# Kernel tuning notes

Hardware: AMD Instinct MI355X
Metric: run time of the kernel (lower is better)

## Reference

```python
import jax, jax.numpy as jnp
import numpy as np

INPUT_DIM = 1024
NUM_CLASSES = 1024
NUM_EXPERTS = 8
TOP_K = 2
HIDDEN = 128  # hard-coded in Expert


def setup_inputs() -> dict:
    key = jax.random.key(0)
    ks = jax.random.split(key, 7)
    s = 0.02
    return {
        "x": jax.random.normal(ks[0], (16384, INPUT_DIM), dtype=jnp.float32),
        "gate_w": jax.random.normal(ks[1], (INPUT_DIM, NUM_EXPERTS), dtype=jnp.float32) * s,
        "gate_b": jnp.zeros((NUM_EXPERTS,), dtype=jnp.float32),
        "w1": jax.random.normal(ks[2], (NUM_EXPERTS, INPUT_DIM, HIDDEN), dtype=jnp.float32) * s,
        "b1": jnp.zeros((NUM_EXPERTS, HIDDEN), dtype=jnp.float32),
        "w2": jax.random.normal(ks[3], (NUM_EXPERTS, HIDDEN, NUM_CLASSES), dtype=jnp.float32) * s,
        "b2": jnp.zeros((NUM_EXPERTS, NUM_CLASSES), dtype=jnp.float32),
    }


def reference(x, gate_w, gate_b, w1, b1, w2, b2):
    B = x.shape[0]
    # gating: softmax over experts, then top-k
    scores = jax.nn.softmax(x @ gate_w + gate_b, axis=1)          # [B, E]
    top_vals, top_idx = jax.lax.top_k(scores, TOP_K)              # [B, K]
    # dense all-expert compute (E small, fixed), then gather selected outputs
    h = jax.nn.relu(jnp.einsum('bi,eih->ebh', x, w1) + b1[:, None, :])   # [E, B, H]
    y = jnp.einsum('ebh,ehc->ebc', h, w2) + b2[:, None, :]               # [E, B, C]
    y = jnp.transpose(y, (1, 0, 2))                                      # [B, E, C]
    sel = jnp.take_along_axis(y, top_idx[:, :, None], axis=1)            # [B, K, C]
    output = jnp.sum(top_vals[:, :, None] * sel, axis=1)                 # [B, C]
    # gates expanded to [B, K, C] then summed over batch -> [K, C]
    gates_sum = jnp.broadcast_to(jnp.sum(top_vals, axis=0)[:, None], (TOP_K, NUM_CLASSES))
    return (output, gates_sum)
```

## Files before the change

kernel.cpp:

```cpp
#include <hip/hip_runtime.h>

#define B_ROWS  16384
#define IN_DIM  1024
#define NEXP    8
#define HID     128
#define NCLS    1024
#define NPAIR   56
#define MAXW1   520
#define MAXW2   312

#define GATE_BLOCKS (B_ROWS / 8)
#define W1T_BLOCKS  (NEXP * (IN_DIM / 32) * (HID / 32))
#define W2T_BLOCKS  (NEXP * (HID / 32) * (NCLS / 32))

typedef __attribute__((ext_vector_type(8))) short bf16x8;
typedef __attribute__((ext_vector_type(4))) float f32x4;
typedef __attribute__((ext_vector_type(4))) unsigned int u32x4;
typedef __attribute__((ext_vector_type(8))) unsigned short u16x8;

__device__ __forceinline__ unsigned short f2bf(float f) {
  union { float f; unsigned u; } v; v.f = f;
  unsigned r = v.u + 0x7FFFu + ((v.u >> 16) & 1u);
  return (unsigned short)(r >> 16);
}

__device__ __forceinline__ int sw64(int row, int sh) {
  return (row << 6) + ((((sh >> 3) ^ row) & 7) << 3) + (sh & 7);
}
__device__ __forceinline__ int sw256(int row, int sh) {
  return (row << 8) + ((((sh >> 3) ^ row) & 7) << 3) + (sh & 7) + ((sh >> 6) << 6);
}

__global__ __launch_bounds__(256) void prep_kernel(
    const float* __restrict__ x, const float* __restrict__ gw,
    const float* __restrict__ gb, const float* __restrict__ w1,
    const float* __restrict__ w2, unsigned short* __restrict__ xb,
    unsigned short* __restrict__ w1bt, unsigned short* __restrict__ w2bt,
    float2* __restrict__ tval, unsigned char* __restrict__ pairid) {
  __shared__ __attribute__((aligned(16))) unsigned char pmem[NEXP * IN_DIM * 4];
  const int bid = blockIdx.x;
  const int t = threadIdx.x;

  if (bid < GATE_BLOCKS) {
    float (*gws)[IN_DIM] = (float(*)[IN_DIM])pmem;
#pragma unroll
    for (int kk = 0; kk < 4; ++kk) {
      const int k = kk * 256 + t;
      const float4 g0 = *(const float4*)(gw + k * NEXP);
      const float4 g1 = *(const float4*)(gw + k * NEXP + 4);
      gws[0][k] = g0.x; gws[1][k] = g0.y; gws[2][k] = g0.z; gws[3][k] = g0.w;
      gws[4][k] = g1.x; gws[5][k] = g1.y; gws[6][k] = g1.z; gws[7][k] = g1.w;
    }
    __syncthreads();

    const int wave = t >> 6, l = t & 63;
    const int r0 = bid * 8 + wave * 2;

    float4 xv0[4], xv1[4];
#pragma unroll
    for (int j = 0; j < 4; ++j) {
      xv0[j] = *(const float4*)(x + (size_t)r0 * IN_DIM + j * 256 + l * 4);
      xv1[j] = *(const float4*)(x + (size_t)(r0 + 1) * IN_DIM + j * 256 + l * 4);
    }

    if (xb) {
#pragma unroll
      for (int j = 0; j < 4; ++j) {
        uint2 p0, p1;
        p0.x = (unsigned)f2bf(xv0[j].x) | ((unsigned)f2bf(xv0[j].y) << 16);
        p0.y = (unsigned)f2bf(xv0[j].z) | ((unsigned)f2bf(xv0[j].w) << 16);
        p1.x = (unsigned)f2bf(xv1[j].x) | ((unsigned)f2bf(xv1[j].y) << 16);
        p1.y = (unsigned)f2bf(xv1[j].z) | ((unsigned)f2bf(xv1[j].w) << 16);
        *(uint2*)(xb + (size_t)r0 * IN_DIM + j * 256 + l * 4)       = p0;
        *(uint2*)(xb + (size_t)(r0 + 1) * IN_DIM + j * 256 + l * 4) = p1;
      }
    }

    float a0[NEXP], a1[NEXP];
#pragma unroll
    for (int e = 0; e < NEXP; ++e) { a0[e] = 0.f; a1[e] = 0.f; }
#pragma unroll
    for (int e = 0; e < NEXP; ++e) {
#pragma unroll
      for (int j = 0; j < 4; ++j) {
        const float4 g = *(const float4*)&gws[e][j * 256 + l * 4];
        a0[e] = fmaf(xv0[j].x, g.x, a0[e]); a0[e] = fmaf(xv0[j].y, g.y, a0[e]);
        a0[e] = fmaf(xv0[j].z, g.z, a0[e]); a0[e] = fmaf(xv0[j].w, g.w, a0[e]);
        a1[e] = fmaf(xv1[j].x, g.x, a1[e]); a1[e] = fmaf(xv1[j].y, g.y, a1[e]);
        a1[e] = fmaf(xv1[j].z, g.z, a1[e]); a1[e] = fmaf(xv1[j].w, g.w, a1[e]);
      }
    }
#pragma unroll
    for (int e = 0; e < NEXP; ++e) {
#pragma unroll
      for (int off = 32; off > 0; off >>= 1) {
        a0[e] += __shfl_xor(a0[e], off);
        a1[e] += __shfl_xor(a1[e], off);
      }
    }

    if (l == 0) {
#pragma unroll
      for (int rr = 0; rr < 2; ++rr) {
        const float* a = rr ? a1 : a0;
        float lg[NEXP];
#pragma unroll
        for (int e = 0; e < NEXP; ++e) lg[e] = a[e] + gb[e];
        float m = lg[0];
#pragma unroll
        for (int e = 1; e < NEXP; ++e) m = fmaxf(m, lg[e]);
        float p[NEXP], s = 0.f;
#pragma unroll
        for (int e = 0; e < NEXP; ++e) { p[e] = __expf(lg[e] - m); s += p[e]; }
        const float inv = 1.f / s;
        int   i0 = 0;  float v0 = p[0];
#pragma unroll
        for (int e = 1; e < NEXP; ++e) if (p[e] > v0) { v0 = p[e]; i0 = e; }
        int   i1 = -1; float v1 = -1.f;
#pragma unroll
        for (int e = 0; e < NEXP; ++e)
          if (e != i0 && p[e] > v1) { v1 = p[e]; i1 = e; }
        tval[r0 + rr] = make_float2(v0 * inv, v1 * inv);
        pairid[r0 + rr] = (unsigned char)(i0 * 7 + i1 - (i1 > i0 ? 1 : 0));
      }
    }
  } else {
    float (*tile)[33] = (float(*)[33])pmem;
    const float* src; unsigned short* dst;
    int R, C, r0, c0, e;
    if (bid < GATE_BLOCKS + W1T_BLOCKS) {
      const int b1 = bid - GATE_BLOCKS;
      e = b1 >> 7; const int rem = b1 & 127;
      R = IN_DIM; C = HID;
      c0 = (rem & 3) * 32; r0 = (rem >> 2) * 32;
      src = w1; dst = w1bt;
    } else {
      const int b2 = bid - GATE_BLOCKS - W1T_BLOCKS;
      e = b2 >> 7; const int rem = b2 & 127;
      R = HID; C = NCLS;
      c0 = (rem & 31) * 32; r0 = (rem >> 5) * 32;
      src = w2; dst = w2bt;
    }
    src += (size_t)e * R * C;
    dst += (size_t)e * R * C;
    const int tx = t & 31, ty = t >> 5;
#pragma unroll
    for (int i = ty; i < 32; i += 8)
      tile[i][tx] = src[(size_t)(r0 + i) * C + c0 + tx];
    __syncthreads();
#pragma unroll
    for (int i = ty; i < 32; i += 8)
      dst[(size_t)(c0 + i) * R + r0 + tx] = f2bf(tile[tx][i]);
  }
}

__global__ __launch_bounds__(256) void hist_part_kernel(
    const unsigned char* __restrict__ pairid, const float2* __restrict__ tval,
    int* __restrict__ partials, float2* __restrict__ psum) {
  __shared__ int h[64];
  __shared__ float s0a[256], s1a[256];
  const int t = threadIdx.x;
  if (t < 64) h[t] = 0;
  __syncthreads();
  const int row = blockIdx.x * 256 + t;
  const int p  = pairid[row];
  const int ea = p / 7, rem = p % 7;
  const int eb = rem + (rem >= ea ? 1 : 0);
  atomicAdd(&h[p], 1);
  atomicAdd(&h[56 + ea], 1);
  atomicAdd(&h[56 + eb], 1);
  const float2 v = tval[row];
  s0a[t] = v.x; s1a[t] = v.y;
  __syncthreads();
#pragma unroll
  for (int s = 128; s > 0; s >>= 1) {
    if (t < s) { s0a[t] += s0a[t + s]; s1a[t] += s1a[t + s]; }
    __syncthreads();
  }
  if (t < 64) partials[blockIdx.x * 64 + t] = h[t];
  if (t == 0) psum[blockIdx.x] = make_float2(s0a[0], s1a[0]);
}

__global__ void scan_kernel(const int* __restrict__ partials,
                            const float2* __restrict__ psum,
                            int* __restrict__ hist, int* __restrict__ base,
                            int* __restrict__ csr, int* __restrict__ meta,
                            float* __restrict__ out) {
  const int t = threadIdx.x;
  __shared__ float gg[2];
  if (t < 64) {
    int s = 0;
    for (int b = 0; b < B_ROWS / 256; ++b) s += partials[b * 64 + t];
    hist[t] = s;
  }
  if (t == 0) {
    float g0 = 0.f, g1 = 0.f;
    for (int b = 0; b < B_ROWS / 256; ++b) { g0 += psum[b].x; g1 += psum[b].y; }
    gg[0] = g0; gg[1] = g1;
  }
  __syncthreads();
  float* gout = out + (size_t)B_ROWS * NCLS;
  for (int c = t; c < NCLS; c += 64) {
    gout[c]        = gg[0];
    gout[NCLS + c] = gg[1];
  }
  if (t != 0) return;
  int accp = 0, acce = 0;
  for (int p = 0; p < NPAIR; ++p) { base[p] = accp; csr[p] = accp; accp += hist[p]; }
  for (int e = 0; e < NEXP; ++e) {
    base[56 + e] = acce; csr[56 + e] = acce; acce += hist[56 + e];
  }
  int n = 0;
  int* w1 = meta + 2;
  for (int e = 0; e < NEXP; ++e) {
    const int tiles = (hist[56 + e] + 63) >> 6;
    for (int i = 0; i < tiles; ++i) w1[n++] = (e << 16) | i;
  }
  meta[0] = n;
  n = 0;
  int* w2 = meta + 2 + MAXW1;
  for (int p = 0; p < NPAIR; ++p) {
    const int tiles = (hist[p] + 63) >> 6;
    for (int i = 0; i < tiles; ++i) w2[n++] = (p << 16) | i;
  }
  meta[1] = n;
}

__global__ __launch_bounds__(256) void scatter_kernel(
    const unsigned char* __restrict__ pairid, int* __restrict__ csr,
    int* __restrict__ elist, int* __restrict__ plist) {
  __shared__ int h[64], lbase[64];
  const int t = threadIdx.x;
  if (t < 64) h[t] = 0;
  __syncthreads();
  const int row = blockIdx.x * 256 + t;
  const int p  = pairid[row];
  const int ea = p / 7, rem = p % 7;
  const int eb = rem + (rem >= ea ? 1 : 0);
  const int op = atomicAdd(&h[p], 1);
  const int oa = atomicAdd(&h[56 + ea], 1);
  const int ob = atomicAdd(&h[56 + eb], 1);
  __syncthreads();
  if (t < 64) lbase[t] = h[t] ? atomicAdd(&csr[t], h[t]) : 0;
  __syncthreads();
  const int pp = lbase[p] + op;
  plist[pp] = row;
  elist[lbase[56 + ea] + oa] = (pp << 15) | (row << 1);
  elist[lbase[56 + eb] + ob] = (pp << 15) | (row << 1) | 1;
}

template <bool XB>
__global__ __launch_bounds__(256) void k1_hidden(
    const float* __restrict__ x, const unsigned short* __restrict__ xb,
    const unsigned short* __restrict__ w1bt, const float* __restrict__ b1,
    const float2* __restrict__ tval, const int* __restrict__ elist,
    const int* __restrict__ hist, const int* __restrict__ base,
    const int* __restrict__ meta, unsigned short* __restrict__ Hg) {
  const int b = blockIdx.x;
  if (b >= meta[0]) return;
  const int item = meta[2 + b];
  const int e = item >> 16, tile = item & 0xffff;
  const int start = tile * 64;
  const int nr = min(64, hist[56 + e] - start);

  __shared__ unsigned short As[64 * 64];
  __shared__ unsigned short Bs[128 * 64];
  __shared__ int rowl[64];

  const int t = threadIdx.x;
  if (t < 64) rowl[t] = elist[base[56 + e] + start + (t < nr ? t : 0)];
  __syncthreads();

  const int wid = t >> 6, l = t & 63;
  const int wr = wid >> 1, wc = wid & 1;
  const int lg = l >> 4,   ln = l & 15;

  f32x4 acc[2][4];
#pragma unroll
  for (int ms = 0; ms < 2; ++ms)
#pragma unroll
    for (int nf = 0; nf < 4; ++nf) acc[ms][nf] = (f32x4){0.f, 0.f, 0.f, 0.f};

  const int ai = t >> 2, aseg = t & 3;
  const int arow = (rowl[ai] >> 1) & 0x3FFF;
  const float* asrcf = x + (size_t)arow * IN_DIM + aseg * 16;
  const unsigned short* asrcb = xb + (size_t)arow * IN_DIM + aseg * 16;
  const int bn = t >> 1, bhf = t & 1;
  const unsigned short* bsrc =
      w1bt + ((size_t)e * HID + bn) * IN_DIM + bhf * 32;

  if constexpr (XB) {
    u32x4 areg[2], breg[4];
    {
      const u32x4* ap = (const u32x4*)(asrcb);
      areg[0] = ap[0]; areg[1] = ap[1];
      const u32x4* bp = (const u32x4*)(bsrc);
#pragma unroll
      for (int j = 0; j < 4; ++j) breg[j] = bp[j];
    }
    for (int ks = 0; ks < 16; ++ks) {
      *(u32x4*)&As[sw64(ai, aseg * 16)]     = areg[0];
      *(u32x4*)&As[sw64(ai, aseg * 16 + 8)] = areg[1];
#pragma unroll
      for (int j = 0; j < 4; ++j)
        *(u32x4*)&Bs[sw64(bn, bhf * 32 + j * 8)] = breg[j];
      __syncthreads();
      if (ks < 15) {
        const u32x4* ap = (const u32x4*)(asrcb + (ks + 1) * 64);
        areg[0] = ap[0]; areg[1] = ap[1];
        const u32x4* bp = (const u32x4*)(bsrc + (ks + 1) * 64);
#pragma unroll
        for (int j = 0; j < 4; ++j) breg[j] = bp[j];
      }
      bf16x8 af[2][2], bf[4][2];
#pragma unroll
      for (int ms = 0; ms < 2; ++ms)
#pragma unroll
        for (int kh = 0; kh < 2; ++kh)
          af[ms][kh] = *(const bf16x8*)&As[sw64(wr*32 + ms*16 + ln, kh*32 + lg*8)];
#pragma unroll
      for (int nf = 0; nf < 4; ++nf)
#pragma unroll
        for (int kh = 0; kh < 2; ++kh)
          bf[nf][kh] = *(const bf16x8*)&Bs[sw64(wc*64 + nf*16 + ln, kh*32 + lg*8)];
#pragma unroll
      for (int ms = 0; ms < 2; ++ms)
#pragma unroll
        for (int nf = 0; nf < 4; ++nf) {
          acc[ms][nf] = __builtin_amdgcn_mfma_f32_16x16x32_bf16(af[ms][0], bf[nf][0], acc[ms][nf], 0, 0, 0);
          acc[ms][nf] = __builtin_amdgcn_mfma_f32_16x16x32_bf16(af[ms][1], bf[nf][1], acc[ms][nf], 0, 0, 0);
        }
      __syncthreads();
    }
  } else {
    for (int ks = 0; ks < 16; ++ks) {
      {
        const float4 f0 = *(const float4*)(asrcf + ks * 64);
        const float4 f1 = *(const float4*)(asrcf + ks * 64 + 4);
        const float4 f2 = *(const float4*)(asrcf + ks * 64 + 8);
        const float4 f3 = *(const float4*)(asrcf + ks * 64 + 12);
        u16x8 u0, u1;
        u0[0]=f2bf(f0.x); u0[1]=f2bf(f0.y); u0[2]=f2bf(f0.z); u0[3]=f2bf(f0.w);
        u0[4]=f2bf(f1.x); u0[5]=f2bf(f1.y); u0[6]=f2bf(f1.z); u0[7]=f2bf(f1.w);
        u1[0]=f2bf(f2.x); u1[1]=f2bf(f2.y); u1[2]=f2bf(f2.z); u1[3]=f2bf(f2.w);
        u1[4]=f2bf(f3.x); u1[5]=f2bf(f3.y); u1[6]=f2bf(f3.z); u1[7]=f2bf(f3.w);
        *(u16x8*)&As[sw64(ai, aseg * 16)]     = u0;
        *(u16x8*)&As[sw64(ai, aseg * 16 + 8)] = u1;
      }
      {
        const u32x4* bp = (const u32x4*)(bsrc + ks * 64);
#pragma unroll
        for (int j = 0; j < 4; ++j)
          *(u32x4*)&Bs[sw64(bn, bhf * 32 + j * 8)] = bp[j];
      }
      __syncthreads();
      bf16x8 af[2][2], bf[4][2];
#pragma unroll
      for (int ms = 0; ms < 2; ++ms)
#pragma unroll
        for (int kh = 0; kh < 2; ++kh)
          af[ms][kh] = *(const bf16x8*)&As[sw64(wr*32 + ms*16 + ln, kh*32 + lg*8)];
#pragma unroll
      for (int nf = 0; nf < 4; ++nf)
#pragma unroll
        for (int kh = 0; kh < 2; ++kh)
          bf[nf][kh] = *(const bf16x8*)&Bs[sw64(wc*64 + nf*16 + ln, kh*32 + lg*8)];
#pragma unroll
      for (int ms = 0; ms < 2; ++ms)
#pragma unroll
        for (int nf = 0; nf < 4; ++nf) {
          acc[ms][nf] = __builtin_amdgcn_mfma_f32_16x16x32_bf16(af[ms][0], bf[nf][0], acc[ms][nf], 0, 0, 0);
          acc[ms][nf] = __builtin_amdgcn_mfma_f32_16x16x32_bf16(af[ms][1], bf[nf][1], acc[ms][nf], 0, 0, 0);
        }
      __syncthreads();
    }
  }

  float b1c[4];
#pragma unroll
  for (int nf = 0; nf < 4; ++nf) b1c[nf] = b1[e * HID + wc*64 + nf*16 + ln];

#pragma unroll
  for (int ms = 0; ms < 2; ++ms)
#pragma unroll
    for (int r = 0; r < 4; ++r) {
      const int li = wr*32 + ms*16 + lg*4 + r;
      if (li < nr) {
        const int packed = rowl[li];
        const int row  = (packed >> 1) & 0x3FFF;
        const int slot = packed & 1;
        const int pp   = ((unsigned)packed) >> 15;
        const float2 tv = tval[row];
        const float vv = slot ? tv.y : tv.x;
#pragma unroll
        for (int nf = 0; nf < 4; ++nf) {
          const float hh = fmaxf(acc[ms][nf][r] + b1c[nf], 0.f) * vv;
          Hg[((size_t)pp * 2 + slot) * HID + wc*64 + nf*16 + ln] = f2bf(hh);
        }
      }
    }
}

__global__ __launch_bounds__(256) void k2_out(
    const unsigned short* __restrict__ Hg, const unsigned short* __restrict__ w2bt,
    const float* __restrict__ b2, const float2* __restrict__ tval,
    const int* __restrict__ plist, const int* __restrict__ hist,
    const int* __restrict__ base, const int* __restrict__ meta,
    float* __restrict__ out) {
  const int b = blockIdx.y;
  if (b >= meta[1]) return;
  const int item = meta[2 + MAXW1 + b];
  const int p = item >> 16, rt = item & 0xffff;
  const int ea = p / 7, rem = p % 7;
  const int eb = rem + (rem >= ea ? 1 : 0);
  const int start = rt * 64;
  const int gpos = base[p] + start;
  const int nr = min(64, hist[p] - start);
  const int c0 = blockIdx.x * 128;

  __shared__ unsigned short Ah[64 * 256];
  __shared__ unsigned short Bs[128 * 64];
  __shared__ int rowl[64];
  __shared__ float2 vals[64];

  const int t = threadIdx.x;
  if (t < 64) {
    const int r = plist[gpos + (t < nr ? t : 0)];
    rowl[t] = r;
    vals[t] = tval[r];
  }
  __syncthreads();

  {
    const int i = t >> 2, q = t & 3;
    const int srow = min(gpos + i, B_ROWS - 1);
    const u32x4* src = (const u32x4*)(Hg + (size_t)srow * 256 + q * 64);
#pragma unroll
    for (int j = 0; j < 8; ++j)
      *(u32x4*)&Ah[sw256(i, q * 64 + j * 8)] = src[j];
  }

  const int wid = t >> 6, l = t & 63;
  const int wr = wid >> 1, wc = wid & 1;
  const int lg = l >> 4,   ln = l & 15;

  f32x4 acc[2][4];
#pragma unroll
  for (int ms = 0; ms < 2; ++ms)
#pragma unroll
    for (int nf = 0; nf < 4; ++nf) acc[ms][nf] = (f32x4){0.f, 0.f, 0.f, 0.f};

  const int bn = t >> 1, bhf = t & 1;
  u32x4 breg[4];
  {
    const u32x4* bp = (const u32x4*)(
        w2bt + ((size_t)ea * NCLS + c0 + bn) * HID + bhf * 32);
#pragma unroll
    for (int j = 0; j < 4; ++j) breg[j] = bp[j];
  }
#pragma unroll
  for (int ks = 0; ks < 4; ++ks) {
#pragma unroll
    for (int j = 0; j < 4; ++j)
      *(u32x4*)&Bs[sw64(bn, bhf * 32 + j * 8)] = breg[j];
    __syncthreads();
    if (ks < 3) {
      const int exn = (ks + 1 < 2) ? ea : eb;
      const int hbn = ((ks + 1) & 1) * 64;
      const u32x4* bp = (const u32x4*)(
          w2bt + ((size_t)exn * NCLS + c0 + bn) * HID + hbn + bhf * 32);
#pragma unroll
      for (int j = 0; j < 4; ++j) breg[j] = bp[j];
    }
    bf16x8 af[2][2], bf[4][2];
#pragma unroll
    for (int ms = 0; ms < 2; ++ms)
#pragma unroll
      for (int kh = 0; kh < 2; ++kh)
        af[ms][kh] = *(const bf16x8*)&Ah[sw256(wr*32 + ms*16 + ln, ks*64 + kh*32 + lg*8)];
#pragma unroll
    for (int nf = 0; nf < 4; ++nf)
#pragma unroll
      for (int kh = 0; kh < 2; ++kh)
        bf[nf][kh] = *(const bf16x8*)&Bs[sw64(wc*64 + nf*16 + ln, kh*32 + lg*8)];
#pragma unroll
    for (int ms = 0; ms < 2; ++ms)
#pragma unroll
      for (int nf = 0; nf < 4; ++nf) {
        acc[ms][nf] = __builtin_amdgcn_mfma_f32_16x16x32_bf16(af[ms][0], bf[nf][0], acc[ms][nf], 0, 0, 0);
        acc[ms][nf] = __builtin_amdgcn_mfma_f32_16x16x32_bf16(af[ms][1], bf[nf][1], acc[ms][nf], 0, 0, 0);
      }
    __syncthreads();
  }

  float b2a[4], b2b[4];
#pragma unroll
  for (int nf = 0; nf < 4; ++nf) {
    const int c = c0 + wc*64 + nf*16 + ln;
    b2a[nf] = b2[ea * NCLS + c];
    b2b[nf] = b2[eb * NCLS + c];
  }
#pragma unroll
  for (int ms = 0; ms < 2; ++ms)
#pragma unroll
    for (int r = 0; r < 4; ++r) {
      const int li = wr*32 + ms*16 + lg*4 + r;
      if (li < nr) {
        const int row = rowl[li];
        const float2 v = vals[li];
#pragma unroll
        for (int nf = 0; nf < 4; ++nf) {
          const int c = c0 + wc*64 + nf*16 + ln;
          out[(size_t)row * NCLS + c] = acc[ms][nf][r] + v.x * b2a[nf] + v.y * b2b[nf];
        }
      }
    }
}

extern "C" void kernel_launch(void* const* d_in, const int* in_sizes, int n_in,
                              void* d_out, int out_size, void* d_ws, size_t ws_size,
                              hipStream_t stream) {
  const float* x   = (const float*)d_in[0];
  const float* gw  = (const float*)d_in[1];
  const float* gb  = (const float*)d_in[2];
  const float* w1  = (const float*)d_in[3];
  const float* b1  = (const float*)d_in[4];
  const float* w2  = (const float*)d_in[5];
  const float* b2  = (const float*)d_in[6];
  float* out = (float*)d_out;

  char* ws = (char*)d_ws;
  int*            hist     = (int*)(ws);
  int*            base     = (int*)(ws + 256);
  int*            csr      = (int*)(ws + 512);
  int*            meta     = (int*)(ws + 768);
  int*            partials = (int*)(ws + 4352);
  float2*         psum     = (float2*)(ws + 20736);
  unsigned char*  pairid   = (unsigned char*)(ws + 21248);
  float2*         tval     = (float2*)(ws + 37632);
  int*            elist    = (int*)(ws + 168704);
  int*            plist    = (int*)(ws + 299776);
  unsigned short* w1bt     = (unsigned short*)(ws + 365312);
  unsigned short* w2bt     = (unsigned short*)(ws + 2462464);
  unsigned short* Hg       = (unsigned short*)(ws + 4559616);
  const bool use_xb = (ws_size >= (size_t)46502656);
  unsigned short* xb = use_xb ? (unsigned short*)(ws + 12948224) : nullptr;

  prep_kernel<<<GATE_BLOCKS + W1T_BLOCKS + W2T_BLOCKS, 256, 0, stream>>>(
      x, gw, gb, w1, w2, xb, w1bt, w2bt, tval, pairid);
  hist_part_kernel<<<B_ROWS / 256, 256, 0, stream>>>(pairid, tval, partials, psum);
  scan_kernel<<<1, 64, 0, stream>>>(partials, psum, hist, base, csr, meta, out);
  scatter_kernel<<<B_ROWS / 256, 256, 0, stream>>>(pairid, csr, elist, plist);

  if (use_xb)
    k1_hidden<true><<<MAXW1, 256, 0, stream>>>(x, xb, w1bt, b1, tval, elist,
                                               hist, base, meta, Hg);
  else
    k1_hidden<false><<<MAXW1, 256, 0, stream>>>(x, xb, w1bt, b1, tval, elist,
                                                hist, base, meta, Hg);
  k2_out<<<dim3(NCLS / 128, MAXW2), 256, 0, stream>>>(Hg, w2bt, b2, tval, plist,
                                                      hist, base, meta, out);
}
```

Measured before the change: 119.2 us.

## Fuse histogram into gating kernel, parallelize scan, widen k2 column tiles

Measured after the change: 187.4 us. 57.2% more time.

```diff
diff --git a/kernel.cpp b/kernel.cpp
--- a/kernel.cpp
+++ b/kernel.cpp
@@ -36,8 +36,11 @@
     const float* __restrict__ gb, const float* __restrict__ w1,
     const float* __restrict__ w2, unsigned short* __restrict__ xb,
     unsigned short* __restrict__ w1bt, unsigned short* __restrict__ w2bt,
-    float2* __restrict__ tval, unsigned char* __restrict__ pairid) {
+    float2* __restrict__ tval, unsigned char* __restrict__ pairid,
+    int* __restrict__ partials, float2* __restrict__ psum) {
   __shared__ __attribute__((aligned(16))) unsigned char pmem[NEXP * IN_DIM * 4];
+  __shared__ int hh[64];
+  __shared__ float ps[8];
   const int bid = blockIdx.x;
   const int t = threadIdx.x;
 
@@ -51,6 +54,7 @@
       gws[0][k] = g0.x; gws[1][k] = g0.y; gws[2][k] = g0.z; gws[3][k] = g0.w;
       gws[4][k] = g1.x; gws[5][k] = g1.y; gws[6][k] = g1.z; gws[7][k] = g1.w;
     }
+    if (t < 64) hh[t] = 0;
     __syncthreads();
 
     const int wave = t >> 6, l = t & 63;
@@ -100,6 +104,7 @@
     }
 
     if (l == 0) {
+      float sv0 = 0.f, sv1 = 0.f;
 #pragma unroll
       for (int rr = 0; rr < 2; ++rr) {
         const float* a = rr ? a1 : a0;
@@ -121,9 +126,21 @@
         for (int e = 0; e < NEXP; ++e)
           if (e != i0 && p[e] > v1) { v1 = p[e]; i1 = e; }
         tval[r0 + rr] = make_float2(v0 * inv, v1 * inv);
-        pairid[r0 + rr] = (unsigned char)(i0 * 7 + i1 - (i1 > i0 ? 1 : 0));
-      }
-    }
+        const int pr = i0 * 7 + i1 - (i1 > i0 ? 1 : 0);
+        pairid[r0 + rr] = (unsigned char)pr;
+        sv0 += v0 * inv; sv1 += v1 * inv;
+        atomicAdd(&hh[pr], 1);
+        atomicAdd(&hh[56 + i0], 1);
+        atomicAdd(&hh[56 + i1], 1);
+      }
+      ps[wave * 2]     = sv0;
+      ps[wave * 2 + 1] = sv1;
+    }
+    __syncthreads();
+    if (t < 64) partials[(size_t)bid * 64 + t] = hh[t];
+    if (t == 0)
+      psum[bid] = make_float2(ps[0] + ps[2] + ps[4] + ps[6],
+                              ps[1] + ps[3] + ps[5] + ps[7]);
   } else {
     float (*tile)[33] = (float(*)[33])pmem;
     const float* src; unsigned short* dst;
@@ -154,53 +171,39 @@
   }
 }
 
-__global__ __launch_bounds__(256) void hist_part_kernel(
-    const unsigned char* __restrict__ pairid, const float2* __restrict__ tval,
-    int* __restrict__ partials, float2* __restrict__ psum) {
-  __shared__ int h[64];
-  __shared__ float s0a[256], s1a[256];
+__global__ __launch_bounds__(256) void scan_kernel(
+    const int* __restrict__ partials, const float2* __restrict__ psum,
+    int* __restrict__ hist, int* __restrict__ base, int* __restrict__ csr,
+    int* __restrict__ meta, float* __restrict__ out) {
   const int t = threadIdx.x;
-  if (t < 64) h[t] = 0;
-  __syncthreads();
-  const int row = blockIdx.x * 256 + t;
-  const int p  = pairid[row];
-  const int ea = p / 7, rem = p % 7;
-  const int eb = rem + (rem >= ea ? 1 : 0);
-  atomicAdd(&h[p], 1);
-  atomicAdd(&h[56 + ea], 1);
-  atomicAdd(&h[56 + eb], 1);
-  const float2 v = tval[row];
-  s0a[t] = v.x; s1a[t] = v.y;
-  __syncthreads();
+  __shared__ int hpart[256];
+  __shared__ float r0a[256], r1a[256];
+  __shared__ float gg[2];
+
+  {
+    const int bin = t & 63, ch = t >> 6;
+    int s = 0;
+    for (int b = ch; b < GATE_BLOCKS; b += 4) s += partials[(size_t)b * 64 + bin];
+    hpart[t] = s;
+  }
+  {
+    float g0 = 0.f, g1 = 0.f;
+    for (int b = t; b < GATE_BLOCKS; b += 256) { g0 += psum[b].x; g1 += psum[b].y; }
+    r0a[t] = g0; r1a[t] = g1;
+  }
+  __syncthreads();
+  if (t < 64)
+    hist[t] = hpart[t] + hpart[64 + t] + hpart[128 + t] + hpart[192 + t];
 #pragma unroll
   for (int s = 128; s > 0; s >>= 1) {
-    if (t < s) { s0a[t] += s0a[t + s]; s1a[t] += s1a[t + s]; }
+    if (t < s) { r0a[t] += r0a[t + s]; r1a[t] += r1a[t + s]; }
     __syncthreads();
   }
-  if (t < 64) partials[blockIdx.x * 64 + t] = h[t];
-  if (t == 0) psum[blockIdx.x] = make_float2(s0a[0], s1a[0]);
-}
-
-__global__ void scan_kernel(const int* __restrict__ partials,
-                            const float2* __restrict__ psum,
-                            int* __restrict__ hist, int* __restrict__ base,
-                            int* __restrict__ csr, int* __restrict__ meta,
-                            float* __restrict__ out) {
-  const int t = threadIdx.x;
-  __shared__ float gg[2];
-  if (t < 64) {
-    int s = 0;
-    for (int b = 0; b < B_ROWS / 256; ++b) s += partials[b * 64 + t];
-    hist[t] = s;
-  }
-  if (t == 0) {
-    float g0 = 0.f, g1 = 0.f;
-    for (int b = 0; b < B_ROWS / 256; ++b) { g0 += psum[b].x; g1 += psum[b].y; }
-    gg[0] = g0; gg[1] = g1;
-  }
-  __syncthreads();
+  if (t == 0) { gg[0] = r0a[0]; gg[1] = r1a[0]; }
+  __syncthreads();
+
   float* gout = out + (size_t)B_ROWS * NCLS;
-  for (int c = t; c < NCLS; c += 64) {
+  for (int c = t; c < NCLS; c += 256) {
     gout[c]        = gg[0];
     gout[NCLS + c] = gg[1];
   }
@@ -416,7 +419,7 @@
   const int start = rt * 64;
   const int gpos = base[p] + start;
   const int nr = min(64, hist[p] - start);
-  const int c0 = blockIdx.x * 128;
+  const int c0base = blockIdx.x * 256;
 
   __shared__ unsigned short Ah[64 * 256];
   __shared__ unsigned short Bs[128 * 64];
@@ -443,78 +446,83 @@
   const int wid = t >> 6, l = t & 63;
   const int wr = wid >> 1, wc = wid & 1;
   const int lg = l >> 4,   ln = l & 15;
-
-  f32x4 acc[2][4];
-#pragma unroll
-  for (int ms = 0; ms < 2; ++ms)
-#pragma unroll
-    for (int nf = 0; nf < 4; ++nf) acc[ms][nf] = (f32x4){0.f, 0.f, 0.f, 0.f};
-
   const int bn = t >> 1, bhf = t & 1;
-  u32x4 breg[4];
-  {
-    const u32x4* bp = (const u32x4*)(
-        w2bt + ((size_t)ea * NCLS + c0 + bn) * HID + bhf * 32);
-#pragma unroll
-    for (int j = 0; j < 4; ++j) breg[j] = bp[j];
-  }
-#pragma unroll
-  for (int ks = 0; ks < 4; ++ks) {
-#pragma unroll
-    for (int j = 0; j < 4; ++j)
-      *(u32x4*)&Bs[sw64(bn, bhf * 32 + j * 8)] = breg[j];
-    __syncthreads();
-    if (ks < 3) {
-      const int exn = (ks + 1 < 2) ? ea : eb;
-      const int hbn = ((ks + 1) & 1) * 64;
+
+#pragma unroll
+  for (int ch2 = 0; ch2 < 2; ++ch2) {
+    const int c0 = c0base + ch2 * 128;
+
+    f32x4 acc[2][4];
+#pragma unroll
+    for (int ms = 0; ms < 2; ++ms)
+#pragma unroll
+      for (int nf = 0; nf < 4; ++nf) acc[ms][nf] = (f32x4){0.f, 0.f, 0.f, 0.f};
+
+    u32x4 breg[4];
+    {
       const u32x4* bp = (const u32x4*)(
-          w2bt + ((size_t)exn * NCLS + c0 + bn) * HID + hbn + bhf * 32);
+          w2bt + ((size_t)ea * NCLS + c0 + bn) * HID + bhf * 32);
 #pragma unroll
       for (int j = 0; j < 4; ++j) breg[j] = bp[j];
     }
-    bf16x8 af[2][2], bf[4][2];
+#pragma unroll
+    for (int ks = 0; ks < 4; ++ks) {
+#pragma unroll
+      for (int j = 0; j < 4; ++j)
+        *(u32x4*)&Bs[sw64(bn, bhf * 32 + j * 8)] = breg[j];
+      __syncthreads();
+      if (ks < 3) {
+        const int exn = (ks + 1 < 2) ? ea : eb;
+        const int hbn = ((ks + 1) & 1) * 64;
+        const u32x4* bp = (const u32x4*)(
+            w2bt + ((size_t)exn * NCLS + c0 + bn) * HID + hbn + bhf * 32);
+#pragma unroll
+        for (int j = 0; j < 4; ++j) breg[j] = bp[j];
+      }
+      bf16x8 af[2][2], bf[4][2];
+#pragma unroll
+      for (int ms = 0; ms < 2; ++ms)
+#pragma unroll
+        for (int kh = 0; kh < 2; ++kh)
+          af[ms][kh] = *(const bf16x8*)&Ah[sw256(wr*32 + ms*16 + ln, ks*64 + kh*32 + lg*8)];
+#pragma unroll
+      for (int nf = 0; nf < 4; ++nf)
+#pragma unroll
+        for (int kh = 0; kh < 2; ++kh)
+          bf[nf][kh] = *(const bf16x8*)&Bs[sw64(wc*64 + nf*16 + ln, kh*32 + lg*8)];
+#pragma unroll
+      for (int ms = 0; ms < 2; ++ms)
+#pragma unroll
+        for (int nf = 0; nf < 4; ++nf) {
+          acc[ms][nf] = __builtin_amdgcn_mfma_f32_16x16x32_bf16(af[ms][0], bf[nf][0], acc[ms][nf], 0, 0, 0);
+          acc[ms][nf] = __builtin_amdgcn_mfma_f32_16x16x32_bf16(af[ms][1], bf[nf][1], acc[ms][nf], 0, 0, 0);
+        }
+      __syncthreads();
+    }
+
+    float b2a[4], b2b[4];
+#pragma unroll
+    for (int nf = 0; nf < 4; ++nf) {
+      const int c = c0 + wc*64 + nf*16 + ln;
+      b2a[nf] = b2[ea * NCLS + c];
+      b2b[nf] = b2[eb * NCLS + c];
+    }
 #pragma unroll
     for (int ms = 0; ms < 2; ++ms)
 #pragma unroll
-      for (int kh = 0; kh < 2; ++kh)
-        af[ms][kh] = *(const bf16x8*)&Ah[sw256(wr*32 + ms*16 + ln, ks*64 + kh*32 + lg*8)];
-#pragma unroll
-    for (int nf = 0; nf < 4; ++nf)
-#pragma unroll
-      for (int kh = 0; kh < 2; ++kh)
-        bf[nf][kh] = *(const bf16x8*)&Bs[sw64(wc*64 + nf*16 + ln, kh*32 + lg*8)];
-#pragma unroll
-    for (int ms = 0; ms < 2; ++ms)
-#pragma unroll
-      for (int nf = 0; nf < 4; ++nf) {
-        acc[ms][nf] = __builtin_amdgcn_mfma_f32_16x16x32_bf16(af[ms][0], bf[nf][0], acc[ms][nf], 0, 0, 0);
-        acc[ms][nf] = __builtin_amdgcn_mfma_f32_16x16x32_bf16(af[ms][1], bf[nf][1], acc[ms][nf], 0, 0, 0);
-      }
-    __syncthreads();
-  }
-
-  float b2a[4], b2b[4];
-#pragma unroll
-  for (int nf = 0; nf < 4; ++nf) {
-    const int c = c0 + wc*64 + nf*16 + ln;
-    b2a[nf] = b2[ea * NCLS + c];
-    b2b[nf] = b2[eb * NCLS + c];
-  }
-#pragma unroll
-  for (int ms = 0; ms < 2; ++ms)
-#pragma unroll
-    for (int r = 0; r < 4; ++r) {
-      const int li = wr*32 + ms*16 + lg*4 + r;
-      if (li < nr) {
-        const int row = rowl[li];
-        const float2 v = vals[li];
-#pragma unroll
-        for (int nf = 0; nf < 4; ++nf) {
-          const int c = c0 + wc*64 + nf*16 + ln;
-          out[(size_t)row * NCLS + c] = acc[ms][nf][r] + v.x * b2a[nf] + v.y * b2b[nf];
+      for (int r = 0; r < 4; ++r) {
+        const int li = wr*32 + ms*16 + lg*4 + r;
+        if (li < nr) {
+          const int row = rowl[li];
+          const float2 v = vals[li];
+#pragma unroll
+          for (int nf = 0; nf < 4; ++nf) {
+            const int c = c0 + wc*64 + nf*16 + ln;
+            out[(size_t)row * NCLS + c] = acc[ms][nf][r] + v.x * b2a[nf] + v.y * b2b[nf];
+          }
         }
       }
-    }
+  }
 }
 
 extern "C" void kernel_launch(void* const* d_in, const int* in_sizes, int n_in,
@@ -535,21 +543,20 @@
   int*            csr      = (int*)(ws + 512);
   int*            meta     = (int*)(ws + 768);
   int*            partials = (int*)(ws + 4352);
-  float2*         psum     = (float2*)(ws + 20736);
-  unsigned char*  pairid   = (unsigned char*)(ws + 21248);
-  float2*         tval     = (float2*)(ws + 37632);
-  int*            elist    = (int*)(ws + 168704);
-  int*            plist    = (int*)(ws + 299776);
-  unsigned short* w1bt     = (unsigned short*)(ws + 365312);
-  unsigned short* w2bt     = (unsigned short*)(ws + 2462464);
-  unsigned short* Hg       = (unsigned short*)(ws + 4559616);
-  const bool use_xb = (ws_size >= (size_t)46502656);
-  unsigned short* xb = use_xb ? (unsigned short*)(ws + 12948224) : nullptr;
+  float2*         psum     = (float2*)(ws + 528640);
+  unsigned char*  pairid   = (unsigned char*)(ws + 545024);
+  float2*         tval     = (float2*)(ws + 561408);
+  int*            elist    = (int*)(ws + 692480);
+  int*            plist    = (int*)(ws + 823552);
+  unsigned short* w1bt     = (unsigned short*)(ws + 889088);
+  unsigned short* w2bt     = (unsigned short*)(ws + 2986240);
+  unsigned short* Hg       = (unsigned short*)(ws + 5083392);
+  const bool use_xb = (ws_size >= (size_t)47026432);
+  unsigned short* xb = use_xb ? (unsigned short*)(ws + 13472000) : nullptr;
 
   prep_kernel<<<GATE_BLOCKS + W1T_BLOCKS + W2T_BLOCKS, 256, 0, stream>>>(
-      x, gw, gb, w1, w2, xb, w1bt, w2bt, tval, pairid);
-  hist_part_kernel<<<B_ROWS / 256, 256, 0, stream>>>(pairid, tval, partials, psum);
-  scan_kernel<<<1, 64, 0, stream>>>(partials, psum, hist, base, csr, meta, out);
+      x, gw, gb, w1, w2, xb, w1bt, w2bt, tval, pairid, partials, psum);
+  scan_kernel<<<1, 256, 0, stream>>>(partials, psum, hist, base, csr, meta, out);
   scatter_kernel<<<B_ROWS / 256, 256, 0, stream>>>(pairid, csr, elist, plist);
 
   if (use_xb)
@@ -558,6 +565,6 @@
   else
     k1_hidden<false><<<MAXW1, 256, 0, stream>>>(x, xb, w1bt, b1, tval, elist,
                                                 hist, base, meta, Hg);
-  k2_out<<<dim3(NCLS / 128, MAXW2), 256, 0, stream>>>(Hg, w2bt, b2, tval, plist,
+  k2_out<<<dim3(NCLS / 256, MAXW2), 256, 0, stream>>>(Hg, w2bt, b2, tval, plist,
                                                       hist, base, meta, out);
 }
```
